# Kernel optimization log

Measured on AMD Instinct MI355X. Metric: run time of the kernel, lower is better.

Reference implementation:

```python
import jax, jax.numpy as jnp
import numpy as np

N_ATOMS = 5000
N_EDGES = 100000
F = 128          # num_features
B = 20           # num_basis (sinc expansion)
L = 3            # num_interactions
CUTOFF = 5.0
NUM_EMB = 119


def setup_inputs() -> dict:
    key = jax.random.key(0)
    ks = jax.random.split(key, 16)
    Z = jax.random.randint(ks[0], (N_ATOMS,), 1, NUM_EMB)
    edge_idx = jax.random.randint(ks[1], (N_EDGES, 2), 0, N_ATOMS)
    edge_dist = jax.random.uniform(ks[2], (N_EDGES,), minval=0.5, maxval=6.0, dtype=jnp.float32)
    u = jax.random.normal(ks[3], (N_EDGES, 3), dtype=jnp.float32)
    u = u / jnp.linalg.norm(u, axis=-1, keepdims=True)
    edge_diff = u * edge_dist[:, None]  # displacement vectors with |d| == edge_dist
    s = lambda k, shape: (jax.random.normal(k, shape, dtype=jnp.float32) * 0.05)
    inp = dict(Z=Z, edge_idx=edge_idx, edge_diff=edge_diff, edge_dist=edge_dist)
    inp.update(
        emb=s(ks[4], (NUM_EMB, F)),
        msg_w1=s(ks[5], (L, F, F)), msg_b1=jnp.zeros((L, F), jnp.float32),
        msg_w2=s(ks[6], (L, F, 3 * F)), msg_b2=jnp.zeros((L, 3 * F), jnp.float32),
        filt_w=s(ks[7], (L, B, 3 * F)), filt_b=jnp.zeros((L, 3 * F), jnp.float32),
        upd_U=s(ks[8], (L, F, F)), upd_V=s(ks[9], (L, F, F)),
        upd_w1=s(ks[10], (L, 2 * F, F)), upd_b1=jnp.zeros((L, F), jnp.float32),
        upd_w2=s(ks[11], (L, F, 3 * F)), upd_b2=jnp.zeros((L, 3 * F), jnp.float32),
        ro_w1=s(ks[12], (F, F // 2)), ro_b1=jnp.zeros((F // 2,), jnp.float32),
        ro_w2=s(ks[13], (F // 2, 1)), ro_b2=jnp.zeros((1,), jnp.float32),
    )
    return inp


def _painn(Z, edge_idx, edge_diff, edge_dist,
           emb, msg_w1, msg_b1, msg_w2, msg_b2, filt_w, filt_b,
           upd_U, upd_V, upd_w1, upd_b1, upd_w2, upd_b2,
           ro_w1, ro_b1, ro_w2, ro_b2):
    dtype = edge_diff.dtype
    # edge mask (equivalent to boolean compaction: masked edges contribute 0)
    mask = (edge_dist < CUTOFF).astype(dtype)
    dst = edge_idx[:, 0]  # receiver (index_add target)
    src = edge_idx[:, 1]  # sender (gathered neighbor)
    # sinc radial expansion: sin(n*pi*r/rc)/r, n = 1..B
    n = jnp.arange(1, B + 1, dtype=dtype)
    rbf = jnp.sin(edge_dist[:, None] * n * (jnp.pi / CUTOFF)) / edge_dist[:, None]  # [E,B]
    # cosine cutoff envelope, zeroed outside cutoff
    fc = 0.5 * (jnp.cos(jnp.pi * edge_dist / CUTOFF) + 1.0)
    env = (fc * mask)[:, None]  # [E,1]
    unit = edge_diff / edge_dist[:, None]  # [E,3]

    s_feat = emb[Z]                                   # [N,F]
    v_feat = jnp.zeros((Z.shape[0], 3, F), dtype)     # [N,3,F]

    for l in range(L):
        # ---- PainnMessage ----
        filt = (rbf @ filt_w[l] + filt_b[l]) * env                           # [E,3F]
        phi = jax.nn.silu(s_feat @ msg_w1[l] + msg_b1[l]) @ msg_w2[l] + msg_b2[l]  # [N,3F]
        fo = filt * phi[src]                                                  # [E,3F]
        gsv, gev, ms = jnp.split(fo, 3, axis=-1)                              # each [E,F]
        mv = v_feat[src] * gsv[:, None, :] + gev[:, None, :] * unit[:, :, None]  # [E,3,F]
        s_feat = s_feat + jnp.zeros_like(s_feat).at[dst].add(ms)
        v_feat = v_feat + jnp.zeros_like(v_feat).at[dst].add(mv)
        # ---- PainnUpdate ----
        Uv = jnp.einsum('nif,fg->nig', v_feat, upd_U[l])   # [N,3,F]
        Vv = jnp.einsum('nif,fg->nig', v_feat, upd_V[l])   # [N,3,F]
        Vn = jnp.linalg.norm(Vv, axis=1)                   # [N,F]
        a = jax.nn.silu(jnp.concatenate([s_feat, Vn], axis=-1) @ upd_w1[l] + upd_b1[l]) @ upd_w2[l] + upd_b2[l]
        avv, asv, ass = jnp.split(a, 3, axis=-1)
        v_feat = v_feat + avv[:, None, :] * Uv
        s_feat = s_feat + asv * jnp.sum(Uv * Vv, axis=1) + ass

    # atomwise readout MLP -> per-atom energy
    atom_energy = (jax.nn.silu(s_feat @ ro_w1 + ro_b1) @ ro_w2 + ro_b2)[:, 0]  # [N]
    return atom_energy


def reference(Z, edge_idx, edge_diff, edge_dist,
              emb, msg_w1, msg_b1, msg_w2, msg_b2, filt_w, filt_b,
              upd_U, upd_V, upd_w1, upd_b1, upd_w2, upd_b2,
              ro_w1, ro_b1, ro_w2, ro_b2):
    return _painn(Z, edge_idx, edge_diff, edge_dist,
                  emb, msg_w1, msg_b1, msg_w2, msg_b2, filt_w, filt_b,
                  upd_U, upd_V, upd_w1, upd_b1, upd_w2, upd_b2,
                  ro_w1, ro_b1, ro_w2, ro_b2)
```

## Files before the change

### kernel.cpp

```cpp
#include <hip/hip_runtime.h>
#include <hip/hip_bf16.h>
#include <hip/hip_fp16.h>
#include <math.h>

#define N_ATOMS 5000
#define N_EDGES 100000
#define F 128
#define B 20
#define NL 3
#define CAP 64

constexpr float CUTOFF = 5.0f;
constexpr float PI_F = 3.14159265358979323846f;

typedef _Float16 f16x8 __attribute__((ext_vector_type(8)));
typedef _Float16 h2 __attribute__((ext_vector_type(2)));
typedef float f32x4 __attribute__((ext_vector_type(4)));

struct EMeta { int src; float env; float u0, u1, u2; int pad[3]; };
struct __align__(4) U3 { unsigned int x, y, z; };

__device__ __forceinline__ float silu_f(float x) { return x / (1.0f + __expf(-x)); }

#define PV_IDX(atom, t) (((size_t)(atom) * F + (t)) * 6)

#define NB_INIT 2500
#define NB_BUCK 391

struct TPlanT { const float* src; _Float16* dst; int R, C, pad, blk0, tpc; };
struct TPlansT { TPlanT p[22]; int n; };

__global__ __launch_bounds__(256) void prep_kernel(
    const int* __restrict__ Z, const float* __restrict__ emb,
    float* __restrict__ s, _Float16* __restrict__ s_h,
    float* __restrict__ v, _Float16* __restrict__ pv,
    const int* __restrict__ eidx, int* __restrict__ count, int* __restrict__ bucket,
    TPlansT P) {
    __shared__ float tile[32][33];
    int b = blockIdx.x, tid = threadIdx.x;
    if (b < NB_INIT) {
        int atom = b * 2 + (tid >> 7);
        int t = tid & 127;
        float val = emb[Z[atom] * F + t];
        s[(size_t)atom * F + t] = val;
        s_h[(size_t)atom * F + t] = (_Float16)val;
#pragma unroll
        for (int d = 0; d < 3; ++d) v[((size_t)atom * 3 + d) * F + t] = 0.0f;
        unsigned int* pp = (unsigned int*)(pv + PV_IDX(atom, t));
        pp[0] = 0u; pp[1] = 0u; pp[2] = 0u;
        return;
    }
    if (b < NB_INIT + NB_BUCK) {
        int e = (b - NB_INIT) * 256 + tid;
        if (e < N_EDGES) {
            int dst = eidx[2 * e];
            int pos = atomicAdd(&count[dst], 1);
            if (pos < CAP) bucket[dst * CAP + pos] = e;
        }
        return;
    }
    int tb = b - (NB_INIT + NB_BUCK);
    int pi = 0;
#pragma unroll
    for (int i = 1; i < 22; ++i)
        if (i < P.n && tb >= P.p[i].blk0) pi = i;
    const float* src = P.p[pi].src;
    _Float16* dst = P.p[pi].dst;
    int R = P.p[pi].R, C = P.p[pi].C, pad = P.p[pi].pad;
    int tl = tb - P.p[pi].blk0;
    int tpc = P.p[pi].tpc;
    int tr0 = (tl / tpc) * 32, tc0 = (tl % tpc) * 32;
    int i = tid >> 5, j = tid & 31;
#pragma unroll
    for (int rr = 0; rr < 4; ++rr) {
        int r = tr0 + i + 8 * rr, c = tc0 + j;
        if (r < R && c < C) tile[i + 8 * rr][j] = src[(size_t)r * C + c];
    }
    __syncthreads();
#pragma unroll
    for (int rr = 0; rr < 4; ++rr) {
        int c = tc0 + i + 8 * rr, r = tr0 + j;
        if (c < C && r < R) dst[(size_t)c * pad + r] = (_Float16)tile[j][i + 8 * rr];
    }
}

#define NB_META 1250

__global__ __launch_bounds__(256) void meta_phi_kernel(
    const int* __restrict__ count, const int* __restrict__ bucket,
    const int* __restrict__ eidx, const float* __restrict__ ediff,
    const float* __restrict__ edist,
    EMeta* __restrict__ meta, _Float16* __restrict__ rbfh,
    const _Float16* __restrict__ s_h, const _Float16* __restrict__ w1T,
    const float* __restrict__ b1, const _Float16* __restrict__ w2T,
    const float* __restrict__ b2, _Float16* __restrict__ pv) {
    __shared__ __align__(16) _Float16 shA[16 * 136];
    __shared__ __align__(16) _Float16 shH[16 * 136];
    int b = blockIdx.x, tid = threadIdx.x;
    if (b < NB_META) {
        int slot = b * 256 + tid;
        int a = slot >> 6, i = slot & (CAP - 1);
        if (i >= count[a]) return;
        int e = bucket[slot];
        float d = edist[e];
        EMeta m;
        m.src = eidx[2 * e + 1];
        float theta = d * (PI_F / CUTOFF);
        float s1 = __sinf(theta), c1 = __cosf(theta);
        float fc = 0.5f * (c1 + 1.0f);
        m.env = (d < CUTOFF) ? fc : 0.0f;
        float inv = 1.0f / d;
        m.u0 = ediff[3 * e + 0] * inv;
        m.u1 = ediff[3 * e + 1] * inv;
        m.u2 = ediff[3 * e + 2] * inv;
        m.pad[0] = m.pad[1] = m.pad[2] = 0;
        meta[slot] = m;
        _Float16* rp = rbfh + (size_t)slot * 24;
        float twoc = 2.0f * c1;
        float skm2 = 0.0f, skm1 = s1;
        rp[0] = (_Float16)(s1 * inv);
#pragma unroll
        for (int k = 2; k <= B; ++k) {
            float sk = twoc * skm1 - skm2;
            skm2 = skm1; skm1 = sk;
            rp[k - 1] = (_Float16)(sk * inv);
        }
        rp[20] = rp[21] = rp[22] = rp[23] = (_Float16)0.0f;
        return;
    }
    int r0 = (b - NB_META) * 16;
    {
        int r = tid >> 4, c8 = (tid & 15) * 8;
        int rg = r0 + r; if (rg >= N_ATOMS) rg = N_ATOMS - 1;
        *(f16x8*)(shA + r * 136 + c8) = *(const f16x8*)(s_h + (size_t)rg * F + c8);
    }
    __syncthreads();
    int lane = tid & 63, wv = tid >> 6;
    int col = lane & 15, quad = lane >> 4;
    for (int nt = wv; nt < 8; nt += 4) {
        int n = nt * 16 + col;
        f32x4 acc = {0.f, 0.f, 0.f, 0.f};
#pragma unroll
        for (int kt = 0; kt < 4; ++kt) {
            f16x8 afr = *(const f16x8*)(shA + col * 136 + kt * 32 + quad * 8);
            f16x8 bfr = *(const f16x8*)(w1T + (size_t)n * 128 + kt * 32 + quad * 8);
            acc = __builtin_amdgcn_mfma_f32_16x16x32_f16(afr, bfr, acc, 0, 0, 0);
        }
        float bb = b1[n];
#pragma unroll
        for (int r = 0; r < 4; ++r)
            shH[(quad * 4 + r) * 136 + n] = (_Float16)silu_f(acc[r] + bb);
    }
    __syncthreads();
    for (int nt = wv; nt < 24; nt += 4) {
        int n = nt * 16 + col;
        f32x4 acc = {0.f, 0.f, 0.f, 0.f};
#pragma unroll
        for (int kt = 0; kt < 4; ++kt) {
            f16x8 afr = *(const f16x8*)(shH + col * 136 + kt * 32 + quad * 8);
            f16x8 bfr = *(const f16x8*)(w2T + (size_t)n * 128 + kt * 32 + quad * 8);
            acc = __builtin_amdgcn_mfma_f32_16x16x32_f16(afr, bfr, acc, 0, 0, 0);
        }
        float bb = b2[n];
#pragma unroll
        for (int r = 0; r < 4; ++r) {
            int row = r0 + quad * 4 + r;
            if (row < N_ATOMS)
                pv[PV_IDX(row, n & 127) + (n >> 7)] = (_Float16)(acc[r] + bb);
        }
    }
}

__global__ __launch_bounds__(256) void agg_kernel(
    const int* __restrict__ count, const EMeta* __restrict__ meta,
    const _Float16* __restrict__ rbfh,
    const _Float16* __restrict__ fwT, const float* __restrict__ fb,
    const _Float16* __restrict__ pv_r,
    float* __restrict__ s, float* __restrict__ v,
    _Float16* __restrict__ vmid_h) {
    int a = blockIdx.x;
    int tid = threadIdx.x;
    int t = tid & 127, team = tid >> 7;

    unsigned int frw0[10], frw1[10], frw2[10];
    {
        const unsigned int* p0 = (const unsigned int*)(fwT + (size_t)t * 24);
        const unsigned int* p1 = (const unsigned int*)(fwT + (size_t)(F + t) * 24);
        const unsigned int* p2 = (const unsigned int*)(fwT + (size_t)(2 * F + t) * 24);
#pragma unroll
        for (int j = 0; j < 10; ++j) { frw0[j] = p0[j]; frw1[j] = p1[j]; frw2[j] = p2[j]; }
    }
    float fb0 = fb[t], fb1 = fb[F + t], fb2 = fb[2 * F + t];

    __shared__ int sh_src[CAP];
    __shared__ float sh_env[CAP];
    __shared__ float sh_unit[CAP][3];
    __shared__ __align__(16) unsigned int sh_rbf[CAP * 12];
    __shared__ float sh_part[4][F];

    int n = count[a]; if (n > CAP) n = CAP;
    const size_t aC = (size_t)a * CAP;
    if (tid < n) {
        EMeta m = meta[aC + tid];
        sh_src[tid] = m.src;
        sh_env[tid] = m.env;
        sh_unit[tid][0] = m.u0; sh_unit[tid][1] = m.u1; sh_unit[tid][2] = m.u2;
    }
    const unsigned int* rbf32 = (const unsigned int*)rbfh;
    for (int task = tid; task < n * 12; task += 256) {
        int i = task / 12, w = task - i * 12;
        sh_rbf[i * 12 + w] = rbf32[(aC + i) * 12 + w];
    }
    __syncthreads();

    float accS = 0.f, accV0 = 0.f, accV1 = 0.f, accV2 = 0.f;
    int myCnt = (n > team) ? ((n - team + 1) >> 1) : 0;
    if (myCnt > 0) {
        U3 QA[4], QB[4];
        int ngrp = (myCnt + 3) >> 2;
        auto load_grp = [&](int gbase, U3 Q[4]) {
#pragma unroll
            for (int j = 0; j < 4; ++j) {
                int i = gbase + j;
                int ii = (i < myCnt) ? i : (myCnt - 1);
                int src = sh_src[team + 2 * ii];
                Q[j] = *(const U3*)(pv_r + PV_IDX(src, t));
            }
        };
        auto comp_grp = [&](int gbase, U3 Q[4]) {
#pragma unroll
            for (int j = 0; j < 4; ++j) {
                int i = gbase + j;
                if (i < myCnt) {
                    int ei = team + 2 * i;
                    const uint4* rq = (const uint4*)(sh_rbf + ei * 12);
                    uint4 qa = rq[0], qb = rq[1];
                    uint2 qc = *(const uint2*)(sh_rbf + ei * 12 + 8);
                    unsigned int rr[10] = {qa.x, qa.y, qa.z, qa.w,
                                           qb.x, qb.y, qb.z, qb.w, qc.x, qc.y};
                    float f0 = fb0, f1 = fb1, f2 = fb2;
#pragma unroll
                    for (int p = 0; p < 10; ++p) {
                        h2 rb = __builtin_bit_cast(h2, rr[p]);
                        f0 = __builtin_amdgcn_fdot2(rb, __builtin_bit_cast(h2, frw0[p]), f0, false);
                        f1 = __builtin_amdgcn_fdot2(rb, __builtin_bit_cast(h2, frw1[p]), f1, false);
                        f2 = __builtin_amdgcn_fdot2(rb, __builtin_bit_cast(h2, frw2[p]), f2, false);
                    }
                    float env = sh_env[ei];
                    f0 *= env; f1 *= env; f2 *= env;
                    h2 q0 = __builtin_bit_cast(h2, Q[j].x);
                    h2 q1 = __builtin_bit_cast(h2, Q[j].y);
                    h2 q2 = __builtin_bit_cast(h2, Q[j].z);
                    accS += f2 * (float)q1[0];
                    float gsv = f0 * (float)q0[0];
                    float gev = f1 * (float)q0[1];
                    accV0 += (float)q1[1] * gsv + gev * sh_unit[ei][0];
                    accV1 += (float)q2[0] * gsv + gev * sh_unit[ei][1];
                    accV2 += (float)q2[1] * gsv + gev * sh_unit[ei][2];
                }
            }
        };
        load_grp(0, QA);
        for (int g = 0; g < ngrp; g += 2) {
            if (g + 1 < ngrp) load_grp((g + 1) * 4, QB);
            comp_grp(g * 4, QA);
            if (g + 1 < ngrp) {
                if (g + 2 < ngrp) load_grp((g + 2) * 4, QA);
                comp_grp((g + 1) * 4, QB);
            }
        }
    }

    if (team == 1) {
        sh_part[0][t] = accS; sh_part[1][t] = accV0;
        sh_part[2][t] = accV1; sh_part[3][t] = accV2;
    }
    __syncthreads();
    if (team == 0) {
        float sm = s[(size_t)a * F + t] + accS + sh_part[0][t];
        s[(size_t)a * F + t] = sm;
        float vm0 = v[(size_t)a * 3 * F + t] + accV0 + sh_part[1][t];
        float vm1 = v[(size_t)a * 3 * F + F + t] + accV1 + sh_part[2][t];
        float vm2 = v[(size_t)a * 3 * F + 2 * F + t] + accV2 + sh_part[3][t];
        v[(size_t)a * 3 * F + t] = vm0;
        v[(size_t)a * 3 * F + F + t] = vm1;
        v[(size_t)a * 3 * F + 2 * F + t] = vm2;
        vmid_h[(size_t)(a * 3 + 0) * F + t] = (_Float16)vm0;
        vmid_h[(size_t)(a * 3 + 1) * F + t] = (_Float16)vm1;
        vmid_h[(size_t)(a * 3 + 2) * F + t] = (_Float16)vm2;
    }
}

__global__ __launch_bounds__(512) void fused_update_kernel(
    const _Float16* __restrict__ vmid_h, const _Float16* __restrict__ uvT,
    const _Float16* __restrict__ w1T, const float* __restrict__ b1,
    const _Float16* __restrict__ w2T, const float* __restrict__ b2,
    float* __restrict__ s, float* __restrict__ v, _Float16* __restrict__ pv_w,
    const _Float16* __restrict__ nw1T, const float* __restrict__ nb1,
    const _Float16* __restrict__ nw2T, const float* __restrict__ nb2,
    int do_phi,
    const _Float16* __restrict__ roT16, const float* __restrict__ rb1,
    const float* __restrict__ ro_w2p, const float* __restrict__ rb2,
    float* __restrict__ out, int do_ro) {
    __shared__ __align__(16) _Float16 shA[48 * 136];
    __shared__ __align__(16) _Float16 shUV[48 * 264];
    __shared__ __align__(16) _Float16 shCat[16 * 264];
    __shared__ __align__(16) _Float16 shH[16 * 136];
    __shared__ __align__(16) _Float16 shAa[16 * 392];
    _Float16* shS = shA;
    float* shRO = (float*)shAa;
    int a0 = blockIdx.x * 16;
    int r0 = a0 * 3;
    int tid = threadIdx.x;
    for (int slot = tid; slot < 48 * 16; slot += 512) {
        int r = slot >> 4, c8 = (slot & 15) * 8;
        int rg = r0 + r; if (rg >= N_ATOMS * 3) rg = N_ATOMS * 3 - 1;
        *(f16x8*)(shA + r * 136 + c8) = *(const f16x8*)(vmid_h + (size_t)rg * F + c8);
    }
    __syncthreads();
    int lane = tid & 63, wv = tid >> 6;
    int col = lane & 15, quad = lane >> 4;

    for (int j = wv; j < 48; j += 8) {
        int mt = j >> 4, nt = j & 15;
        int n = nt * 16 + col;
        f32x4 acc = {0.f, 0.f, 0.f, 0.f};
#pragma unroll
        for (int kt = 0; kt < 4; ++kt) {
            f16x8 afr = *(const f16x8*)(shA + (mt * 16 + col) * 136 + kt * 32 + quad * 8);
            f16x8 bfr = *(const f16x8*)(uvT + (size_t)n * 128 + kt * 32 + quad * 8);
            acc = __builtin_amdgcn_mfma_f32_16x16x32_f16(afr, bfr, acc, 0, 0, 0);
        }
#pragma unroll
        for (int r = 0; r < 4; ++r)
            shUV[(mt * 16 + quad * 4 + r) * 264 + n] = (_Float16)acc[r];
    }
    __syncthreads();

    for (int p = tid; p < 2048; p += 512) {
        int ai = p >> 7, t = p & 127;
        int atom = a0 + ai;
        int ag = (atom < N_ATOMS) ? atom : N_ATOMS - 1;
        shCat[ai * 264 + t] = (_Float16)s[(size_t)ag * F + t];
        float x0 = (float)shUV[(ai * 3 + 0) * 264 + 128 + t];
        float x1 = (float)shUV[(ai * 3 + 1) * 264 + 128 + t];
        float x2 = (float)shUV[(ai * 3 + 2) * 264 + 128 + t];
        shCat[ai * 264 + 128 + t] = (_Float16)sqrtf(x0 * x0 + x1 * x1 + x2 * x2);
    }
    __syncthreads();

    for (int nt = wv; nt < 8; nt += 8) {
        int n = nt * 16 + col;
        f32x4 acc = {0.f, 0.f, 0.f, 0.f};
#pragma unroll
        for (int kt = 0; kt < 8; ++kt) {
            f16x8 afr = *(const f16x8*)(shCat + col * 264 + kt * 32 + quad * 8);
            f16x8 bfr = *(const f16x8*)(w1T + (size_t)n * 256 + kt * 32 + quad * 8);
            acc = __builtin_amdgcn_mfma_f32_16x16x32_f16(afr, bfr, acc, 0, 0, 0);
        }
        float bb = b1[n];
#pragma unroll
        for (int r = 0; r < 4; ++r)
            shH[(quad * 4 + r) * 136 + n] = (_Float16)silu_f(acc[r] + bb);
    }
    __syncthreads();

    for (int nt = wv; nt < 24; nt += 8) {
        int n = nt * 16 + col;
        f32x4 acc = {0.f, 0.f, 0.f, 0.f};
#pragma unroll
        for (int kt = 0; kt < 4; ++kt) {
            f16x8 afr = *(const f16x8*)(shH + col * 136 + kt * 32 + quad * 8);
            f16x8 bfr = *(const f16x8*)(w2T + (size_t)n * 128 + kt * 32 + quad * 8);
            acc = __builtin_amdgcn_mfma_f32_16x16x32_f16(afr, bfr, acc, 0, 0, 0);
        }
        float bb = b2[n];
#pragma unroll
        for (int r = 0; r < 4; ++r)
            shAa[(quad * 4 + r) * 392 + n] = (_Float16)(acc[r] + bb);
    }
    __syncthreads();

    for (int p = tid; p < 2048; p += 512) {
        int ai = p >> 7, t = p & 127;
        int atom = a0 + ai;
        if (atom >= N_ATOMS) { shS[ai * 136 + t] = (_Float16)0.0f; continue; }
        float avv = (float)shAa[ai * 392 + t];
        float asv = (float)shAa[ai * 392 + 128 + t];
        float ass = (float)shAa[ai * 392 + 256 + t];
        float dot = 0.f;
        _Float16* pvp = pv_w + PV_IDX(atom, t);
#pragma unroll
        for (int d = 0; d < 3; ++d) {
            float u = (float)shUV[(ai * 3 + d) * 264 + t];
            float w = (float)shUV[(ai * 3 + d) * 264 + 128 + t];
            dot += u * w;
            float nv = v[(size_t)atom * 3 * F + d * F + t] + avv * u;
            v[(size_t)atom * 3 * F + d * F + t] = nv;
            pvp[3 + d] = (_Float16)nv;
        }
        float sn = s[(size_t)atom * F + t] + asv * dot + ass;
        s[(size_t)atom * F + t] = sn;
        shS[ai * 136 + t] = (_Float16)sn;
    }

    if (do_phi) {
        __syncthreads();
        for (int nt = wv; nt < 8; nt += 8) {
            int n = nt * 16 + col;
            f32x4 acc = {0.f, 0.f, 0.f, 0.f};
#pragma unroll
            for (int kt = 0; kt < 4; ++kt) {
                f16x8 afr = *(const f16x8*)(shS + col * 136 + kt * 32 + quad * 8);
                f16x8 bfr = *(const f16x8*)(nw1T + (size_t)n * 128 + kt * 32 + quad * 8);
                acc = __builtin_amdgcn_mfma_f32_16x16x32_f16(afr, bfr, acc, 0, 0, 0);
            }
            float bb = nb1[n];
#pragma unroll
            for (int r = 0; r < 4; ++r)
                shH[(quad * 4 + r) * 136 + n] = (_Float16)silu_f(acc[r] + bb);
        }
        __syncthreads();
        for (int nt = wv; nt < 24; nt += 8) {
            int n = nt * 16 + col;
            f32x4 acc = {0.f, 0.f, 0.f, 0.f};
#pragma unroll
            for (int kt = 0; kt < 4; ++kt) {
                f16x8 afr = *(const f16x8*)(shH + col * 136 + kt * 32 + quad * 8);
                f16x8 bfr = *(const f16x8*)(nw2T + (size_t)n * 128 + kt * 32 + quad * 8);
                acc = __builtin_amdgcn_mfma_f32_16x16x32_f16(afr, bfr, acc, 0, 0, 0);
            }
            float bb = nb2[n];
#pragma unroll
            for (int r = 0; r < 4; ++r) {
                int row = a0 + quad * 4 + r;
                if (row < N_ATOMS)
                    pv_w[PV_IDX(row, n & 127) + (n >> 7)] = (_Float16)(acc[r] + bb);
            }
        }
    }

    if (do_ro) {
        __syncthreads();
        if (wv < 4) {
            int n = wv * 16 + col;
            f32x4 acc = {0.f, 0.f, 0.f, 0.f};
#pragma unroll
            for (int kt = 0; kt < 4; ++kt) {
                f16x8 afr = *(const f16x8*)(shS + col * 136 + kt * 32 + quad * 8);
                f16x8 bfr = *(const f16x8*)(roT16 + (size_t)n * 128 + kt * 32 + quad * 8);
                acc = __builtin_amdgcn_mfma_f32_16x16x32_f16(afr, bfr, acc, 0, 0, 0);
            }
            float bb = rb1[n], w2n = ro_w2p[n];
#pragma unroll
            for (int r = 0; r < 4; ++r)
                shRO[(quad * 4 + r) * 68 + n] = silu_f(acc[r] + bb) * w2n;
        }
        __syncthreads();
        if (tid < 16) {
            int atom = a0 + tid;
            if (atom < N_ATOMS) {
                float sum = rb2[0];
#pragma unroll 8
                for (int k = 0; k < 64; ++k) sum += shRO[tid * 68 + k];
                out[atom] = sum;
            }
        }
    }
}

extern "C" void kernel_launch(void* const* d_in, const int* in_sizes, int n_in,
                              void* d_out, int out_size, void* d_ws, size_t ws_size,
                              hipStream_t stream) {
    const int*   Z      = (const int*)d_in[0];
    const int*   eidx   = (const int*)d_in[1];
    const float* ediff  = (const float*)d_in[2];
    const float* edist  = (const float*)d_in[3];
    const float* emb    = (const float*)d_in[4];
    const float* msg_w1 = (const float*)d_in[5];
    const float* msg_b1 = (const float*)d_in[6];
    const float* msg_w2 = (const float*)d_in[7];
    const float* msg_b2 = (const float*)d_in[8];
    const float* filt_w = (const float*)d_in[9];
    const float* filt_b = (const float*)d_in[10];
    const float* upd_U  = (const float*)d_in[11];
    const float* upd_V  = (const float*)d_in[12];
    const float* upd_w1 = (const float*)d_in[13];
    const float* upd_b1 = (const float*)d_in[14];
    const float* upd_w2 = (const float*)d_in[15];
    const float* upd_b2 = (const float*)d_in[16];
    const float* ro_w1  = (const float*)d_in[17];
    const float* ro_b1  = (const float*)d_in[18];
    const float* ro_w2  = (const float*)d_in[19];
    const float* ro_b2  = (const float*)d_in[20];
    float* out = (float*)d_out;

    float* ws = (float*)d_ws;
    float* s   = ws;
    float* v   = s + N_ATOMS * F;
    int* count  = (int*)(v + N_ATOMS * 3 * F);
    int* bucket = count + N_ATOMS;
    EMeta* meta = (EMeta*)(bucket + N_ATOMS * CAP);
    _Float16* rbfh = (_Float16*)(meta + N_ATOMS * CAP);
    _Float16* s_h  = rbfh + (size_t)N_ATOMS * CAP * 24;
    _Float16* vmid_h = s_h + (size_t)N_ATOMS * F;
    _Float16* pvA  = vmid_h + (size_t)N_ATOMS * 3 * F;
    _Float16* pvB  = pvA + (size_t)N_ATOMS * F * 6;
    _Float16* wh   = pvB + (size_t)N_ATOMS * F * 6;

    const int HWL = 16384 + 49152 + 32768 + 32768 + 49152 + 384 * 24;
    _Float16* mw1T = wh;
    _Float16* mw2T = wh + 16384;
    _Float16* uvT  = wh + 65536;
    _Float16* uw1T = wh + 98304;
    _Float16* uw2T = wh + 131072;
    _Float16* fwTl = wh + 180224;
    _Float16* roT16 = wh + (size_t)NL * HWL;

    TPlansT P; int nb = 0, pi = 0;
    auto add = [&](const float* src, _Float16* dst, int R, int C, int pad) {
        int tr = (R + 31) / 32, tc = (C + 31) / 32;
        P.p[pi].src = src; P.p[pi].dst = dst;
        P.p[pi].R = R; P.p[pi].C = C; P.p[pi].pad = pad;
        P.p[pi].blk0 = nb; P.p[pi].tpc = tc;
        nb += tr * tc; ++pi;
    };
    for (int l = 0; l < NL; ++l) {
        add(msg_w1 + l * F * F,     mw1T + (size_t)l * HWL, F, F, F);
        add(msg_w2 + l * F * 3 * F, mw2T + (size_t)l * HWL, F, 3 * F, F);
        add(upd_U  + l * F * F,     uvT  + (size_t)l * HWL, F, F, F);
        add(upd_V  + l * F * F,     uvT  + (size_t)l * HWL + F * F, F, F, F);
        add(upd_w1 + l * 2 * F * F, uw1T + (size_t)l * HWL, 2 * F, F, 2 * F);
        add(upd_w2 + l * F * 3 * F, uw2T + (size_t)l * HWL, F, 3 * F, F);
        add(filt_w + l * B * 3 * F, fwTl + (size_t)l * HWL, B, 3 * F, 24);
    }
    add(ro_w1, roT16, F, 64, F);
    P.n = pi;

    (void)hipMemsetAsync(count, 0, N_ATOMS * sizeof(int), stream);

    prep_kernel<<<NB_INIT + NB_BUCK + nb, 256, 0, stream>>>(
        Z, emb, s, s_h, v, pvA, eidx, count, bucket, P);

    const int GB16 = (N_ATOMS + 15) / 16;
    meta_phi_kernel<<<NB_META + GB16, 256, 0, stream>>>(
        count, bucket, eidx, ediff, edist, meta, rbfh,
        s_h, mw1T, msg_b1, mw2T, msg_b2, pvA);

    _Float16* pr = pvA;
    _Float16* pw = pvB;
    for (int l = 0; l < NL; ++l) {
        int do_phi = (l + 1 < NL);
        int do_ro = (l == NL - 1);
        int ln = do_phi ? (l + 1) : l;
        agg_kernel<<<N_ATOMS, 256, 0, stream>>>(
            count, meta, rbfh,
            fwTl + (size_t)l * HWL, filt_b + l * 3 * F,
            pr, s, v, vmid_h);
        fused_update_kernel<<<GB16, 512, 0, stream>>>(
            vmid_h, uvT + (size_t)l * HWL,
            uw1T + (size_t)l * HWL, upd_b1 + l * F,
            uw2T + (size_t)l * HWL, upd_b2 + l * 3 * F,
            s, v, pw,
            mw1T + (size_t)ln * HWL, msg_b1 + ln * F,
            mw2T + (size_t)ln * HWL, msg_b2 + ln * 3 * F, do_phi,
            roT16, ro_b1, ro_w2, ro_b2, out, do_ro);
        _Float16* tmp = pr; pr = pw; pw = tmp;
    }
}
```

Before: 325.6 us.

## Split agg_kernel edges across four thread teams and stage filter weights in LDS

The per-atom aggregation kernel now runs 512 threads, so four teams of 128 split each atom's edge list instead of two. The partial sums from teams 1-3 are reduced through shared memory by team 0. Filter weights are first copied cooperatively into a shared buffer that is later reused for the edge metadata, and each thread then reads its weights from there instead of strided global loads. Each team now handles fewer edges (about 5 at the average degree of 20), which shortens the serial loop but adds two barriers and more LDS use, and that may reduce occupancy; the prep kernel also drops one redundant zero-store.

```diff
diff --git a/kernel.cpp b/kernel.cpp
--- a/kernel.cpp
+++ b/kernel.cpp
@@ -47,7 +47,7 @@
 #pragma unroll
         for (int d = 0; d < 3; ++d) v[((size_t)atom * 3 + d) * F + t] = 0.0f;
         unsigned int* pp = (unsigned int*)(pv + PV_IDX(atom, t));
-        pp[0] = 0u; pp[1] = 0u; pp[2] = 0u;
+        pp[1] = 0u; pp[2] = 0u;
         return;
     }
     if (b < NB_INIT + NB_BUCK) {
@@ -171,7 +171,7 @@
     }
 }
 
-__global__ __launch_bounds__(256) void agg_kernel(
+__global__ __launch_bounds__(512) void agg_kernel(
     const int* __restrict__ count, const EMeta* __restrict__ meta,
     const _Float16* __restrict__ rbfh,
     const _Float16* __restrict__ fwT, const float* __restrict__ fb,
@@ -182,21 +182,28 @@
     int tid = threadIdx.x;
     int t = tid & 127, team = tid >> 7;
 
+    __shared__ __align__(16) unsigned char shU[18432];
+    __shared__ float sh_part[3][4][F];
+    unsigned int* shFW    = (unsigned int*)shU;
+    int* sh_src           = (int*)shU;
+    float* sh_env         = (float*)(shU + 256);
+    float* sh_unit        = (float*)(shU + 512);
+    unsigned int* sh_rbf  = (unsigned int*)(shU + 1280);
+
+    {
+        const unsigned int* g = (const unsigned int*)fwT;
+        for (int i = tid; i < 4608; i += 512) shFW[i] = g[i];
+    }
+    __syncthreads();
     unsigned int frw0[10], frw1[10], frw2[10];
-    {
-        const unsigned int* p0 = (const unsigned int*)(fwT + (size_t)t * 24);
-        const unsigned int* p1 = (const unsigned int*)(fwT + (size_t)(F + t) * 24);
-        const unsigned int* p2 = (const unsigned int*)(fwT + (size_t)(2 * F + t) * 24);
-#pragma unroll
-        for (int j = 0; j < 10; ++j) { frw0[j] = p0[j]; frw1[j] = p1[j]; frw2[j] = p2[j]; }
+#pragma unroll
+    for (int j = 0; j < 10; ++j) {
+        frw0[j] = shFW[t * 12 + j];
+        frw1[j] = shFW[(128 + t) * 12 + j];
+        frw2[j] = shFW[(256 + t) * 12 + j];
     }
     float fb0 = fb[t], fb1 = fb[F + t], fb2 = fb[2 * F + t];
-
-    __shared__ int sh_src[CAP];
-    __shared__ float sh_env[CAP];
-    __shared__ float sh_unit[CAP][3];
-    __shared__ __align__(16) unsigned int sh_rbf[CAP * 12];
-    __shared__ float sh_part[4][F];
+    __syncthreads();
 
     int n = count[a]; if (n > CAP) n = CAP;
     const size_t aC = (size_t)a * CAP;
@@ -204,17 +211,19 @@
         EMeta m = meta[aC + tid];
         sh_src[tid] = m.src;
         sh_env[tid] = m.env;
-        sh_unit[tid][0] = m.u0; sh_unit[tid][1] = m.u1; sh_unit[tid][2] = m.u2;
+        sh_unit[tid * 3 + 0] = m.u0;
+        sh_unit[tid * 3 + 1] = m.u1;
+        sh_unit[tid * 3 + 2] = m.u2;
     }
     const unsigned int* rbf32 = (const unsigned int*)rbfh;
-    for (int task = tid; task < n * 12; task += 256) {
+    for (int task = tid; task < n * 12; task += 512) {
         int i = task / 12, w = task - i * 12;
         sh_rbf[i * 12 + w] = rbf32[(aC + i) * 12 + w];
     }
     __syncthreads();
 
     float accS = 0.f, accV0 = 0.f, accV1 = 0.f, accV2 = 0.f;
-    int myCnt = (n > team) ? ((n - team + 1) >> 1) : 0;
+    int myCnt = (n > team) ? ((n - team + 3) >> 2) : 0;
     if (myCnt > 0) {
         U3 QA[4], QB[4];
         int ngrp = (myCnt + 3) >> 2;
@@ -223,7 +232,7 @@
             for (int j = 0; j < 4; ++j) {
                 int i = gbase + j;
                 int ii = (i < myCnt) ? i : (myCnt - 1);
-                int src = sh_src[team + 2 * ii];
+                int src = sh_src[team + 4 * ii];
                 Q[j] = *(const U3*)(pv_r + PV_IDX(src, t));
             }
         };
@@ -232,7 +241,7 @@
             for (int j = 0; j < 4; ++j) {
                 int i = gbase + j;
                 if (i < myCnt) {
-                    int ei = team + 2 * i;
+                    int ei = team + 4 * i;
                     const uint4* rq = (const uint4*)(sh_rbf + ei * 12);
                     uint4 qa = rq[0], qb = rq[1];
                     uint2 qc = *(const uint2*)(sh_rbf + ei * 12 + 8);
@@ -254,9 +263,9 @@
                     accS += f2 * (float)q1[0];
                     float gsv = f0 * (float)q0[0];
                     float gev = f1 * (float)q0[1];
-                    accV0 += (float)q1[1] * gsv + gev * sh_unit[ei][0];
-                    accV1 += (float)q2[0] * gsv + gev * sh_unit[ei][1];
-                    accV2 += (float)q2[1] * gsv + gev * sh_unit[ei][2];
+                    accV0 += (float)q1[1] * gsv + gev * sh_unit[ei * 3 + 0];
+                    accV1 += (float)q2[0] * gsv + gev * sh_unit[ei * 3 + 1];
+                    accV2 += (float)q2[1] * gsv + gev * sh_unit[ei * 3 + 2];
                 }
             }
         };
@@ -271,17 +280,23 @@
         }
     }
 
-    if (team == 1) {
-        sh_part[0][t] = accS; sh_part[1][t] = accV0;
-        sh_part[2][t] = accV1; sh_part[3][t] = accV2;
+    if (team != 0) {
+        sh_part[team - 1][0][t] = accS;
+        sh_part[team - 1][1][t] = accV0;
+        sh_part[team - 1][2][t] = accV1;
+        sh_part[team - 1][3][t] = accV2;
     }
     __syncthreads();
     if (team == 0) {
-        float sm = s[(size_t)a * F + t] + accS + sh_part[0][t];
+        float aS  = accS  + sh_part[0][0][t] + sh_part[1][0][t] + sh_part[2][0][t];
+        float aV0 = accV0 + sh_part[0][1][t] + sh_part[1][1][t] + sh_part[2][1][t];
+        float aV1 = accV1 + sh_part[0][2][t] + sh_part[1][2][t] + sh_part[2][2][t];
+        float aV2 = accV2 + sh_part[0][3][t] + sh_part[1][3][t] + sh_part[2][3][t];
+        float sm = s[(size_t)a * F + t] + aS;
         s[(size_t)a * F + t] = sm;
-        float vm0 = v[(size_t)a * 3 * F + t] + accV0 + sh_part[1][t];
-        float vm1 = v[(size_t)a * 3 * F + F + t] + accV1 + sh_part[2][t];
-        float vm2 = v[(size_t)a * 3 * F + 2 * F + t] + accV2 + sh_part[3][t];
+        float vm0 = v[(size_t)a * 3 * F + t] + aV0;
+        float vm1 = v[(size_t)a * 3 * F + F + t] + aV1;
+        float vm2 = v[(size_t)a * 3 * F + 2 * F + t] + aV2;
         v[(size_t)a * 3 * F + t] = vm0;
         v[(size_t)a * 3 * F + F + t] = vm1;
         v[(size_t)a * 3 * F + 2 * F + t] = vm2;
@@ -553,7 +568,7 @@
         int do_phi = (l + 1 < NL);
         int do_ro = (l == NL - 1);
         int ln = do_phi ? (l + 1) : l;
-        agg_kernel<<<N_ATOMS, 256, 0, stream>>>(
+        agg_kernel<<<N_ATOMS, 512, 0, stream>>>(
             count, meta, rbfh,
             fwTl + (size_t)l * HWL, filt_b + l * 3 * F,
             pr, s, v, vmid_h);
```

Result: slower. 396.4 us (+21.7%).
